# Optimization experiments

Hardware: AMD Instinct MI355X
Metric: run time of the kernel (lower is better)

The kernel has to match this reference:

```python
import jax, jax.numpy as jnp
import numpy as np

B, T, D, H = 128, 256, 256, 1024
DEC_STEPS = 59


def _gates(g):
    # torch LSTM gate order: input, forget, cell(g), output
    i, f, gg, o = jnp.split(g, 4, axis=-1)
    return jax.nn.sigmoid(i), jax.nn.sigmoid(f), jnp.tanh(gg), jax.nn.sigmoid(o)


def _cell(x, h, c, W_ih, W_hh, b_ih, b_hh):
    g = x @ W_ih.T + b_ih + h @ W_hh.T + b_hh
    i, f, gg, o = _gates(g)
    c = f * c + i * gg
    h = o * jnp.tanh(c)
    return h, c


def _layer(x, W_ih, W_hh, b_ih, b_hh):
    # x: [B, T, Din] -> outputs [B, T, H], final (h, c)
    b, hdim = x.shape[0], W_hh.shape[1]
    xp = jnp.einsum('btd,gd->btg', x, W_ih) + b_ih  # precompute input proj [B,T,4H]

    def step(carry, xt):
        h, c = carry
        g = xt + h @ W_hh.T + b_hh
        i, f, gg, o = _gates(g)
        c = f * c + i * gg
        h = o * jnp.tanh(c)
        return (h, c), h

    h0 = jnp.zeros((b, hdim), x.dtype)
    (hT, cT), hs = jax.lax.scan(step, (h0, h0), jnp.swapaxes(xp, 0, 1))
    return jnp.swapaxes(hs, 0, 1), hT, cT


def setup_inputs() -> dict:
    key = jax.random.key(0)
    ks = jax.random.split(key, 12)
    s = 1.0 / np.sqrt(H)
    u = lambda k, shape: jax.random.uniform(k, shape, jnp.float32, -s, s)
    return {
        'x': jax.random.normal(ks[0], (B, T, D), jnp.float32),
        'W_ih0': u(ks[1], (4 * H, D)),
        'W_hh0': u(ks[2], (4 * H, H)),
        'b_ih0': u(ks[3], (4 * H,)),
        'b_hh0': u(ks[4], (4 * H,)),
        'W_ih1': u(ks[5], (4 * H, H)),
        'W_hh1': u(ks[6], (4 * H, H)),
        'b_ih1': u(ks[7], (4 * H,)),
        'b_hh1': u(ks[8], (4 * H,)),
        'W_lin': u(ks[9], (D, H)),
        'b_lin': u(ks[10], (D,)),
    }


def reference(x, W_ih0, W_hh0, b_ih0, b_hh0, W_ih1, W_hh1, b_ih1, b_hh1, W_lin, b_lin):
    out0, h0, c0 = _layer(x, W_ih0, W_hh0, b_ih0, b_hh0)
    out1, h1, c1 = _layer(out0, W_ih1, W_hh1, b_ih1, b_hh1)
    y_last = out1[:, -1, :] @ W_lin.T + b_lin  # [B, D]

    def dec(carry, _):
        h0_, c0_, h1_, c1_, y = carry
        h0_, c0_ = _cell(y, h0_, c0_, W_ih0, W_hh0, b_ih0, b_hh0)
        h1_, c1_ = _cell(h0_, h1_, c1_, W_ih1, W_hh1, b_ih1, b_hh1)
        y = h1_ @ W_lin.T + b_lin
        return (h0_, c0_, h1_, c1_, y), y

    _, ys = jax.lax.scan(dec, (h0, c0, h1, c1, y_last), None, length=DEC_STEPS)
    ys = jnp.swapaxes(ys, 0, 1)  # [B, 59, D]
    # original returns y[:, T-1:, :] => last prefix prediction + 59 decoded steps
    return jnp.concatenate([y_last[:, None, :], ys], axis=1)  # [B, 60, D]
```

## Files before the change

kernel.cpp:

```cpp
#include <hip/hip_runtime.h>
#include <hip/hip_bf16.h>
#include <cstdint>


typedef _Float16 half_t;
typedef _Float16 half8 __attribute__((ext_vector_type(8)));
typedef float float4v __attribute__((ext_vector_type(4)));
typedef int int32x4_t __attribute__((ext_vector_type(4)));
typedef float float32x4_t __attribute__((ext_vector_type(4)));

__device__ float32x4_t llvm_amdgcn_raw_buffer_load_fp32x4(
    int32x4_t srsrc, int voffset, int soffset, int aux)
    __asm("llvm.amdgcn.raw.buffer.load.v4f32");

#define AUX_SC1 16

union SrdU { int32x4_t v; struct { const void* p; unsigned nr, fl; } s; };
__device__ __forceinline__ int32x4_t make_srd(const void* p) {
  SrdU u; u.s.p = p; u.s.nr = 0xFFFFFFFFu; u.s.fl = 0x00020000u; return u.v;
}

__device__ __forceinline__ unsigned poll4(const int* p) {
  union { float32x4_t f; int i[4]; } u;
  u.f = llvm_amdgcn_raw_buffer_load_fp32x4(make_srd(p), 0, 0, AUX_SC1);
  unsigned m = 0;
  if (u.i[0] >= 16) m |= 1u;
  if (u.i[1] >= 16) m |= 2u;
  if (u.i[2] >= 16) m |= 4u;
  if (u.i[3] >= 16) m |= 8u;
  return m;
}

__device__ __forceinline__ void wait8(const int* f) {
  for (;;) {
    unsigned m = poll4(f) | (poll4(f + 4) << 4);
    if (m == 0xFFu) return;
    __builtin_amdgcn_s_sleep(2);
  }
}

__device__ __forceinline__ void flag_add(int* p) {
  __hip_atomic_fetch_add(p, 1, __ATOMIC_RELAXED, __HIP_MEMORY_SCOPE_AGENT);
}

__device__ __forceinline__ void gate(const int* f, int tid) {
  if (tid == 0) wait8(f);
  asm volatile("" ::: "memory");
  __builtin_amdgcn_s_barrier();
  asm volatile("" ::: "memory");
}

__device__ __forceinline__ float sigm_(float x) { return 1.0f / (1.0f + __expf(-x)); }
__device__ __forceinline__ float tanh_(float x) {
  float ax = fabsf(x);
  float e = __expf(-2.0f * ax);
  float t = (1.0f - e) / (1.0f + e);
  return x < 0.0f ? -t : t;
}

#define MFMA16(a, b, c) __builtin_amdgcn_mfma_f32_16x16x32_f16(a, b, c, 0, 0, 0)


template <int NC>
__device__ __forceinline__ void issue_chunks(const half_t* __restrict__ A, int ro,
                                             half8 (&a0)[NC][4], half8 (&a1)[NC][4]) {
#pragma unroll
  for (int c = 0; c < NC; ++c)
#pragma unroll
    for (int k4 = 0; k4 < 4; ++k4) {
      const half_t* ap = A + (c * 16 + k4 * 4) * 1024 + ro;
      a0[c][k4] = *(const half8*)ap;
      a1[c][k4] = *(const half8*)(ap + 128);
    }
}

template <int NC>
__device__ __forceinline__ void consume_chunks(const half8 (&a0)[NC][4],
                                               const half8 (&a1)[NC][4],
                                               const half_t* __restrict__ W, int kk0,
                                               int lq, int lrow, float4v acc[2][2]) {
#pragma unroll
  for (int c = 0; c < NC; ++c)
#pragma unroll
    for (int k4 = 0; k4 < 4; ++k4) {
      const half_t* bp = W + (kk0 + c * 4 + k4) * 1024 + lq * 256 + lrow * 8;
      half8 b0 = *(const half8*)bp;
      half8 b1 = *(const half8*)(bp + 128);
      acc[0][0] = MFMA16(a0[c][k4], b0, acc[0][0]);
      acc[0][1] = MFMA16(a0[c][k4], b1, acc[0][1]);
      acc[1][0] = MFMA16(a1[c][k4], b0, acc[1][0]);
      acc[1][1] = MFMA16(a1[c][k4], b1, acc[1][1]);
    }
}

__device__ __forceinline__ void stream_main8(const half_t* __restrict__ A,
                                             const half_t* __restrict__ W, int kk0,
                                             int ro, int lq, int lrow,
                                             float4v acc[2][2],
                                             half8 (&a0)[4][4], half8 (&a1)[4][4]) {
#pragma unroll
  for (int c = 0; c < 8; ++c) {
#pragma unroll
    for (int k4 = 0; k4 < 4; ++k4) {
      const half_t* bp = W + (kk0 + c * 4 + k4) * 1024 + lq * 256 + lrow * 8;
      half8 b0 = *(const half8*)bp;
      half8 b1 = *(const half8*)(bp + 128);
      acc[0][0] = MFMA16(a0[c & 3][k4], b0, acc[0][0]);
      acc[0][1] = MFMA16(a0[c & 3][k4], b1, acc[0][1]);
      acc[1][0] = MFMA16(a1[c & 3][k4], b0, acc[1][0]);
      acc[1][1] = MFMA16(a1[c & 3][k4], b1, acc[1][1]);
    }
    if (c < 4) {
#pragma unroll
      for (int k4 = 0; k4 < 4; ++k4) {
        const half_t* ap = A + ((c + 4) * 16 + k4 * 4) * 1024 + ro;
        a0[c][k4] = *(const half8*)ap;
        a1[c][k4] = *(const half8*)(ap + 128);
      }
    }
  }
}

__device__ __forceinline__ void stream8(const half_t* __restrict__ A,
                                        const half_t* __restrict__ W, int kk0,
                                        int ro, int lq, int lrow, float4v acc[2][2]) {
  half8 a0[4][4], a1[4][4];
  issue_chunks<4>(A, ro, a0, a1);
  stream_main8(A, W, kk0, ro, lq, lrow, acc, a0, a1);
}

__device__ __forceinline__ void stream8_pre2(const half_t* __restrict__ A,
                                             const half_t* __restrict__ W, int kk0,
                                             const half8 (&xa0)[2][4],
                                             const half8 (&xa1)[2][4],
                                             int ro, int lq, int lrow,
                                             float4v acc[2][2]) {
  half8 a0[4][4], a1[4][4];
  issue_chunks<4>(A, ro, a0, a1);
  consume_chunks<2>(xa0, xa1, W, 0, lq, lrow, acc);
  stream_main8(A, W, kk0, ro, lq, lrow, acc, a0, a1);
}

__device__ __forceinline__ void epi_gates(
    float4v acc[2][2], int tile, const float* __restrict__ biasArr,
    float c[2][2], half_t* hTile, half_t* __restrict__ hDst, int tid) {
  const int l = tid & 63, rg = tid >> 6;
  const int lrow = l & 15, lq = l >> 4, q = l & 3, a = lrow >> 2;
#pragma unroll
  for (int m = 0; m < 2; ++m)
#pragma unroll
    for (int nf = 0; nf < 2; ++nf) {
      const float bias = biasArr[tile * 32 + nf * 16 + lrow];
      float gi = 0.f, gf = 0.f, gg = 0.f, go = 0.f;
#pragma unroll
      for (int r = 0; r < 4; ++r) {
        float x = acc[m][nf][r] + bias;
        float t1 = __shfl_xor(x, 1);
        float t2 = __shfl_xor(x, 2);
        float t3 = __shfl_xor(x, 3);
        if (r == q) {
          gi = (q == 0) ? x : (q == 1 ? t1 : (q == 2 ? t2 : t3));
          gf = (q == 1) ? x : (q == 0 ? t1 : (q == 3 ? t2 : t3));
          gg = (q == 2) ? x : (q == 3 ? t1 : (q == 0 ? t2 : t3));
          go = (q == 3) ? x : (q == 2 ? t1 : (q == 1 ? t2 : t3));
        }
      }
      const int row = rg * 32 + m * 16 + lq * 4 + q;
      const int ju = nf * 4 + a;
      float iv = sigm_(gi), fv = sigm_(gf), gv = tanh_(gg), ov = sigm_(go);
      float cnew = fv * c[m][nf] + iv * gv;
      c[m][nf] = cnew;
      hTile[row * 8 + ju] = (half_t)(ov * tanh_(cnew));
    }
  __syncthreads();
  if (tid < 128) {
    const unsigned long long* s = (const unsigned long long*)(hTile + tid * 8);
    unsigned long long v0 = s[0], v1 = s[1];
    unsigned long long* d = (unsigned long long*)(hDst + tid * 8);
    __hip_atomic_store(d, v0, __ATOMIC_RELAXED, __HIP_MEMORY_SCOPE_AGENT);
    __hip_atomic_store(d + 1, v1, __ATOMIC_RELAXED, __HIP_MEMORY_SCOPE_AGENT);
  }
}

__device__ __forceinline__ void epi_y(
    float4v acc[2][2], int ytile, int i, const float* __restrict__ biasY,
    float* __restrict__ out, int tid) {
  const int l = tid & 63, rg = tid >> 6;
  const int lrow = l & 15, lq = l >> 4;
#pragma unroll
  for (int m = 0; m < 2; ++m)
#pragma unroll
    for (int nf = 0; nf < 2; ++nf) {
      const int d = ytile * 32 + nf * 16 + lrow;
      const float b = biasY[d];
#pragma unroll
      for (int r = 0; r < 4; ++r) {
        const int row = rg * 32 + m * 16 + lq * 4 + r;
        out[(long)row * 15360 + i * 256 + d] = acc[m][nf][r] + b;
      }
    }
}

__device__ __forceinline__ void loadW(const half_t* __restrict__ src,
                                      half_t* dst, int halves, int tid) {
  for (int i = tid * 8; i < halves; i += 2048)
    *(uint4*)(dst + i) = *(const uint4*)(src + i);
}

#define ZACC2 float4v acc[2][2]; { float4v z = {0.f, 0.f, 0.f, 0.f}; \
  acc[0][0] = z; acc[0][1] = z; acc[1][0] = z; acc[1][1] = z; }

__global__ void __launch_bounds__(256, 1) k_lstm(
    const half_t* __restrict__ S0, const half_t* __restrict__ S1,
    const half_t* __restrict__ SD, const half_t* __restrict__ SY,
    const half_t* __restrict__ XH,
    half_t* __restrict__ H0, half_t* __restrict__ H1,
    const float* __restrict__ B0P, const float* __restrict__ B1P,
    const float* __restrict__ BD0P, float* __restrict__ out, int* FLG) {
  __shared__ char smem[133120];
  half_t* ldsW = (half_t*)smem;
  half_t* hTile = (half_t*)(smem + 131072);
  const int w = blockIdx.x, tid = threadIdx.x;
  const int l = tid & 63, rg = tid >> 6;
  const int lrow = l & 15, lq = l >> 4;
  const int ro = (rg * 32 + lrow) * 8 + lq * 1024;
  float c2[2][2] = {{0.f, 0.f}, {0.f, 0.f}};
#define SLOTP(base, idx) ((base) + (long)(idx) * 131072)

  if (w < 128) {
    const int g = w >> 4;
    loadW(S0 + (long)w * 40960, ldsW, 40960, tid);
    __syncthreads();
    for (int s = 0; s < 256; ++s) {
      ZACC2;
      half8 xa0[2][4], xa1[2][4];
      issue_chunks<2>(XH + (long)s * 32768, ro, xa0, xa1);
      if (s >= 1) gate(FLG + (s - 1) * 32, tid);
      stream8_pre2(SLOTP(H0, s), ldsW, 8, xa0, xa1, ro, lq, lrow, acc);
      epi_gates(acc, w, B0P, c2, hTile, SLOTP(H0, s + 1) + w * 1024, tid);
      __syncthreads();
      if (tid == 0) flag_add(FLG + s * 32 + g);
    }
    __syncthreads();
    loadW(SD + (long)w * 65536, ldsW, 65536, tid);
    __syncthreads();
    for (int i = 0; i < 59; ++i) {
      ZACC2;
      gate(FLG + (255 + i) * 32, tid);
      stream8(SLOTP(H0, 256 + i), ldsW, 32, ro, lq, lrow, acc);
      gate(FLG + (256 + i) * 32 + 8, tid);
      stream8(SLOTP(H1, 256 + i), ldsW, 0, ro, lq, lrow, acc);
      epi_gates(acc, w, BD0P, c2, hTile, SLOTP(H0, 257 + i) + w * 1024, tid);
      __syncthreads();
      if (tid == 0) flag_add(FLG + (256 + i) * 32 + g);
    }
  } else {
    const int bw = w - 128, g = bw >> 4;
    loadW(S1 + (long)bw * 65536, ldsW, 65536, tid);
    __syncthreads();
    for (int s = 1; s <= 256; ++s) {
      ZACC2;
      if (s >= 2) gate(FLG + (s - 1) * 32 + 8, tid);
      stream8(SLOTP(H1, s - 1), ldsW, 32, ro, lq, lrow, acc);
      gate(FLG + (s - 1) * 32, tid);
      stream8(SLOTP(H0, s), ldsW, 0, ro, lq, lrow, acc);
      epi_gates(acc, bw, B1P, c2, hTile, SLOTP(H1, s) + bw * 1024, tid);
      __syncthreads();
      if (tid == 0) flag_add(FLG + s * 32 + 8 + g);
    }
    for (int i = 0; i < 59; ++i) {
      ZACC2;
      gate(FLG + (256 + i) * 32 + 8, tid);
      stream8(SLOTP(H1, 256 + i), ldsW, 32, ro, lq, lrow, acc);
      gate(FLG + (256 + i) * 32, tid);
      stream8(SLOTP(H0, 257 + i), ldsW, 0, ro, lq, lrow, acc);
      epi_gates(acc, bw, B1P, c2, hTile, SLOTP(H1, 257 + i) + bw * 1024, tid);
      __syncthreads();
      if (tid == 0) flag_add(FLG + (257 + i) * 32 + 8 + g);
    }
  }

  for (int j = w; j < 480; j += 256) {
    const int i = j >> 3, t = j & 7;
    ZACC2;
    gate(FLG + (256 + i) * 32 + 8, tid);
    stream8(SLOTP(H1, 256 + i), SY + (long)t * 32768, 0, ro, lq, lrow, acc);
    epi_y(acc, t, i, BD0P + 4096, out, tid);
  }
#undef SLOTP
}


__global__ void k_cvt_x(const float* __restrict__ x, half_t* __restrict__ XH) {
  int idx = blockIdx.x * 256 + threadIdx.x;
  int t = idx >> 12;
  int kb = (idx >> 7) & 31;
  int r = idx & 127;
  const float* src = x + ((long)((r << 8) + t)) * 256 + kb * 8;
  float4 v0 = *(const float4*)src;
  float4 v1 = *(const float4*)(src + 4);
  half_t tmp[8] = {(half_t)v0.x, (half_t)v0.y, (half_t)v0.z, (half_t)v0.w,
                   (half_t)v1.x, (half_t)v1.y, (half_t)v1.z, (half_t)v1.w};
  *(uint4*)(XH + (long)t * 32768 + kb * 1024 + r * 8) = *(const uint4*)tmp;
}

__global__ void k_pack32(const float* __restrict__ A, int KA,
                         const float* __restrict__ Bsrc,
                         half_t* __restrict__ dst, int KT32, int skipA) {
  int idx = blockIdx.x * 256 + threadIdx.x;
  int nn = idx & 31;
  int lq = (idx >> 5) & 3;
  int t2 = idx >> 7;
  int kk = t2 % KT32;
  int tile = t2 / KT32;
  if (tile >= 128) return;
  int k = kk * 32 + lq * 8;
  int rp = tile * 32 + nn;
  int r = ((rp & 3) << 10) + (rp >> 2);
  const float* src;
  if (k < KA) {
    if (skipA) return;
    src = A + (long)r * KA + k;
  } else {
    src = Bsrc + (long)r * 1024 + (k - KA);
  }
  float4 v0 = *(const float4*)src;
  float4 v1 = *(const float4*)(src + 4);
  half_t tmp[8] = {(half_t)v0.x, (half_t)v0.y, (half_t)v0.z, (half_t)v0.w,
                   (half_t)v1.x, (half_t)v1.y, (half_t)v1.z, (half_t)v1.w};
  *(uint4*)(dst + (long)tile * (KT32 * 1024) + kk * 1024 + lq * 256 + nn * 8) =
      *(const uint4*)tmp;
}

__global__ void k_pack_y32(const float* __restrict__ Wlin,
                           half_t* __restrict__ SY) {
  int idx = blockIdx.x * 256 + threadIdx.x;
  int nn = idx & 31;
  int lq = (idx >> 5) & 3;
  int kk = (idx >> 7) & 31;
  int tile = idx >> 12;
  int d = tile * 32 + nn;
  int k = kk * 32 + lq * 8;
  const float* src = Wlin + (long)d * 1024 + k;
  float4 v0 = *(const float4*)src;
  float4 v1 = *(const float4*)(src + 4);
  half_t tmp[8] = {(half_t)v0.x, (half_t)v0.y, (half_t)v0.z, (half_t)v0.w,
                   (half_t)v1.x, (half_t)v1.y, (half_t)v1.z, (half_t)v1.w};
  *(uint4*)(SY + (long)tile * 32768 + kk * 1024 + lq * 256 + nn * 8) =
      *(const uint4*)tmp;
}

__global__ void k_bias_simple(const float* bi0, const float* bh0,
                              const float* bi1, const float* bh1,
                              const float* blin, float* b0p, float* b1p,
                              float* bD0p) {
  int rp = blockIdx.x * blockDim.x + threadIdx.x;
  if (rp < 4096) {
    int r = ((rp & 3) << 10) + (rp >> 2);
    b0p[rp] = bi0[r] + bh0[r];
    b1p[rp] = bi1[r] + bh1[r];
  } else if (rp < 4352) {
    bD0p[rp] = blin[rp - 4096];
  }
}

__global__ void k_bias_dot(const float* __restrict__ Wih0,
                           const float* __restrict__ blin,
                           const float* __restrict__ bi0,
                           const float* __restrict__ bh0,
                           float* __restrict__ bD0p) {
  int wv = threadIdx.x >> 6, l = threadIdx.x & 63;
  int r = blockIdx.x * 4 + wv;
  float s = 0.f;
#pragma unroll
  for (int c = 0; c < 4; ++c) s += Wih0[r * 256 + c * 64 + l] * blin[c * 64 + l];
#pragma unroll
  for (int o = 32; o >= 1; o >>= 1) s += __shfl_xor(s, o);
  if (l == 0) {
    int rp = ((r & 1023) << 2) | (r >> 10);
    bD0p[rp] = bi0[r] + bh0[r] + s;
  }
}

__global__ void k_weff(const float* __restrict__ Wih0,
                       const float* __restrict__ Wlin,
                       half_t* __restrict__ SD) {
  __shared__ float At[64][65];
  __shared__ float Bt[64][65];
  const int rt = blockIdx.x, jt = blockIdx.y;
  const int tid = threadIdx.x;
  const int tx = tid & 15, ty = tid >> 4;
  float acc[4][4] = {};
  for (int k0 = 0; k0 < 256; k0 += 64) {
    __syncthreads();
#pragma unroll
    for (int i = 0; i < 16; ++i) {
      int lin = tid + 256 * i;
      int rr = lin >> 6, kk = lin & 63;
      At[rr][kk] = Wih0[(rt * 64 + rr) * 256 + k0 + kk];
      Bt[rr][kk] = Wlin[(k0 + rr) * 1024 + jt * 64 + kk];
    }
    __syncthreads();
    for (int kk = 0; kk < 64; ++kk) {
      float a[4], b[4];
#pragma unroll
      for (int i = 0; i < 4; ++i) a[i] = At[ty * 4 + i][kk];
#pragma unroll
      for (int i = 0; i < 4; ++i) b[i] = Bt[kk][tx * 4 + i];
#pragma unroll
      for (int i = 0; i < 4; ++i)
#pragma unroll
        for (int jx = 0; jx < 4; ++jx) acc[i][jx] += a[i] * b[jx];
    }
  }
#pragma unroll
  for (int i = 0; i < 4; ++i) {
    int r = rt * 64 + ty * 4 + i;
    int rp = ((r & 1023) << 2) | (r >> 10);
    int tile = rp >> 5, nn = rp & 31;
#pragma unroll
    for (int jx = 0; jx < 4; ++jx) {
      int j = jt * 64 + tx * 4 + jx;
      SD[(long)tile * 65536 + (j >> 5) * 1024 + ((j >> 3) & 3) * 256 + nn * 8 +
         (j & 7)] = (half_t)acc[i][jx];
    }
  }
}


extern "C" void kernel_launch(void* const* d_in, const int* in_sizes, int n_in,
                              void* d_out, int out_size, void* d_ws, size_t ws_size,
                              hipStream_t stream) {
  (void)in_sizes; (void)n_in; (void)out_size; (void)ws_size;
  const float* x    = (const float*)d_in[0];
  const float* Wih0 = (const float*)d_in[1];
  const float* Whh0 = (const float*)d_in[2];
  const float* bi0  = (const float*)d_in[3];
  const float* bh0  = (const float*)d_in[4];
  const float* Wih1 = (const float*)d_in[5];
  const float* Whh1 = (const float*)d_in[6];
  const float* bi1  = (const float*)d_in[7];
  const float* bh1  = (const float*)d_in[8];
  const float* Wlin = (const float*)d_in[9];
  const float* blin = (const float*)d_in[10];
  float* out = (float*)d_out;
  char* ws = (char*)d_ws;

  half_t* S0  = (half_t*)(ws + 0);
  half_t* S1  = (half_t*)(ws + 10485760);
  half_t* SD  = (half_t*)(ws + 27262976);
  half_t* SY  = (half_t*)(ws + 44040192);
  half_t* XH  = (half_t*)(ws + 44564480);
  float*  B0P = (float*)(ws + 61341696);
  float*  B1P = (float*)(ws + 61358080);
  float*  BD0P= (float*)(ws + 61374464);
  int*    FLG = (int*)(ws + 61391872);
  half_t* H0  = (half_t*)(ws + 61432320);
  half_t* H1  = (half_t*)(ws + 145318400);

  hipMemsetAsync(ws + 61391872, 0, 302592, stream);
  hipMemsetAsync(H1, 0, 262144, stream);

  k_cvt_x<<<4096, 256, 0, stream>>>(x, XH);
  k_bias_simple<<<17, 256, 0, stream>>>(bi0, bh0, bi1, bh1, blin, B0P, B1P, BD0P);
  k_bias_dot<<<1024, 256, 0, stream>>>(Wih0, blin, bi0, bh0, BD0P);
  k_pack32<<<2560, 256, 0, stream>>>(Wih0, 256, Whh0, S0, 40, 0);
  k_pack32<<<4096, 256, 0, stream>>>(Wih1, 1024, Whh1, S1, 64, 0);
  k_pack32<<<4096, 256, 0, stream>>>(nullptr, 1024, Whh0, SD, 64, 1);
  k_pack_y32<<<128, 256, 0, stream>>>(Wlin, SY);
  k_weff<<<dim3(64, 16), 256, 0, stream>>>(Wih0, Wlin, SD);

  k_lstm<<<256, 256, 0, stream>>>(S0, S1, SD, SY, XH, H0, H1,
                                  B0P, B1P, BD0P, out, FLG);
}
```

Measured before the change: 5.521 ms.

## Replace per-group atomic counters with per-block byte flags and early input MFMA

The cross-block step flags change from eight atomic-increment counters per layer-step to a 128-byte record per layer-step. Each block stores one byte with a relaxed store, and the waiter checks all 128 bytes with eight vector buffer loads against 0x01010101. In layer 0, the input-projection MFMAs now run before the gate wait, so that work overlaps the dependency stall. The flag area moves after H1, and H0 slot 0 is now zeroed explicitly. The cost is more polling loads per check and reliance on byte-store visibility ordering relative to the H writes.

```diff
diff --git a/kernel.cpp b/kernel.cpp
--- a/kernel.cpp
+++ b/kernel.cpp
@@ -20,31 +20,31 @@
   SrdU u; u.s.p = p; u.s.nr = 0xFFFFFFFFu; u.s.fl = 0x00020000u; return u.v;
 }
 
-__device__ __forceinline__ unsigned poll4(const int* p) {
-  union { float32x4_t f; int i[4]; } u;
-  u.f = llvm_amdgcn_raw_buffer_load_fp32x4(make_srd(p), 0, 0, AUX_SC1);
-  unsigned m = 0;
-  if (u.i[0] >= 16) m |= 1u;
-  if (u.i[1] >= 16) m |= 2u;
-  if (u.i[2] >= 16) m |= 4u;
-  if (u.i[3] >= 16) m |= 8u;
-  return m;
-}
-
-__device__ __forceinline__ void wait8(const int* f) {
-  for (;;) {
-    unsigned m = poll4(f) | (poll4(f + 4) << 4);
-    if (m == 0xFFu) return;
-    __builtin_amdgcn_s_sleep(2);
-  }
-}
-
-__device__ __forceinline__ void flag_add(int* p) {
-  __hip_atomic_fetch_add(p, 1, __ATOMIC_RELAXED, __HIP_MEMORY_SCOPE_AGENT);
+__device__ __forceinline__ bool poll128(const int* p) {
+  union { float32x4_t f; int i[4]; } u[8];
+  int32x4_t srd = make_srd(p);
+#pragma unroll
+  for (int j = 0; j < 8; ++j)
+    u[j].f = llvm_amdgcn_raw_buffer_load_fp32x4(srd, j * 16, 0, AUX_SC1);
+  int ok = 1;
+#pragma unroll
+  for (int j = 0; j < 8; ++j)
+#pragma unroll
+    for (int k = 0; k < 4; ++k) ok &= (u[j].i[k] == 0x01010101);
+  return ok != 0;
+}
+
+__device__ __forceinline__ void wait128(const int* f) {
+  while (!poll128(f)) __builtin_amdgcn_s_sleep(2);
+}
+
+__device__ __forceinline__ void flag_set(int* recp, int idx) {
+  __hip_atomic_store((char*)recp + idx, (char)1, __ATOMIC_RELAXED,
+                     __HIP_MEMORY_SCOPE_AGENT);
 }
 
 __device__ __forceinline__ void gate(const int* f, int tid) {
-  if (tid == 0) wait8(f);
+  if (tid == 0) wait128(f);
   asm volatile("" ::: "memory");
   __builtin_amdgcn_s_barrier();
   asm volatile("" ::: "memory");
@@ -126,18 +126,6 @@
                                         int ro, int lq, int lrow, float4v acc[2][2]) {
   half8 a0[4][4], a1[4][4];
   issue_chunks<4>(A, ro, a0, a1);
-  stream_main8(A, W, kk0, ro, lq, lrow, acc, a0, a1);
-}
-
-__device__ __forceinline__ void stream8_pre2(const half_t* __restrict__ A,
-                                             const half_t* __restrict__ W, int kk0,
-                                             const half8 (&xa0)[2][4],
-                                             const half8 (&xa1)[2][4],
-                                             int ro, int lq, int lrow,
-                                             float4v acc[2][2]) {
-  half8 a0[4][4], a1[4][4];
-  issue_chunks<4>(A, ro, a0, a1);
-  consume_chunks<2>(xa0, xa1, W, 0, lq, lrow, acc);
   stream_main8(A, W, kk0, ro, lq, lrow, acc, a0, a1);
 }
 
@@ -216,7 +204,7 @@
     const half_t* __restrict__ XH,
     half_t* __restrict__ H0, half_t* __restrict__ H1,
     const float* __restrict__ B0P, const float* __restrict__ B1P,
-    const float* __restrict__ BD0P, float* __restrict__ out, int* FLG) {
+    const float* __restrict__ BD0P, float* __restrict__ out, int* FLGB) {
   __shared__ char smem[133120];
   half_t* ldsW = (half_t*)smem;
   half_t* hTile = (half_t*)(smem + 131072);
@@ -226,67 +214,69 @@
   const int ro = (rg * 32 + lrow) * 8 + lq * 1024;
   float c2[2][2] = {{0.f, 0.f}, {0.f, 0.f}};
 #define SLOTP(base, idx) ((base) + (long)(idx) * 131072)
+#define REC(s, lay) (FLGB + ((((s) * 2 + (lay))) << 6))
 
   if (w < 128) {
-    const int g = w >> 4;
     loadW(S0 + (long)w * 40960, ldsW, 40960, tid);
     __syncthreads();
     for (int s = 0; s < 256; ++s) {
       ZACC2;
       half8 xa0[2][4], xa1[2][4];
       issue_chunks<2>(XH + (long)s * 32768, ro, xa0, xa1);
-      if (s >= 1) gate(FLG + (s - 1) * 32, tid);
-      stream8_pre2(SLOTP(H0, s), ldsW, 8, xa0, xa1, ro, lq, lrow, acc);
+      consume_chunks<2>(xa0, xa1, ldsW, 0, lq, lrow, acc);
+      if (s >= 1) gate(REC(s - 1, 0), tid);
+      stream8(SLOTP(H0, s), ldsW, 8, ro, lq, lrow, acc);
       epi_gates(acc, w, B0P, c2, hTile, SLOTP(H0, s + 1) + w * 1024, tid);
       __syncthreads();
-      if (tid == 0) flag_add(FLG + s * 32 + g);
+      if (tid == 0) flag_set(REC(s, 0), w);
     }
     __syncthreads();
     loadW(SD + (long)w * 65536, ldsW, 65536, tid);
     __syncthreads();
     for (int i = 0; i < 59; ++i) {
       ZACC2;
-      gate(FLG + (255 + i) * 32, tid);
+      gate(REC(255 + i, 0), tid);
       stream8(SLOTP(H0, 256 + i), ldsW, 32, ro, lq, lrow, acc);
-      gate(FLG + (256 + i) * 32 + 8, tid);
+      gate(REC(256 + i, 1), tid);
       stream8(SLOTP(H1, 256 + i), ldsW, 0, ro, lq, lrow, acc);
       epi_gates(acc, w, BD0P, c2, hTile, SLOTP(H0, 257 + i) + w * 1024, tid);
       __syncthreads();
-      if (tid == 0) flag_add(FLG + (256 + i) * 32 + g);
+      if (tid == 0) flag_set(REC(256 + i, 0), w);
     }
   } else {
-    const int bw = w - 128, g = bw >> 4;
+    const int bw = w - 128;
     loadW(S1 + (long)bw * 65536, ldsW, 65536, tid);
     __syncthreads();
     for (int s = 1; s <= 256; ++s) {
       ZACC2;
-      if (s >= 2) gate(FLG + (s - 1) * 32 + 8, tid);
+      if (s >= 2) gate(REC(s - 1, 1), tid);
       stream8(SLOTP(H1, s - 1), ldsW, 32, ro, lq, lrow, acc);
-      gate(FLG + (s - 1) * 32, tid);
+      gate(REC(s - 1, 0), tid);
       stream8(SLOTP(H0, s), ldsW, 0, ro, lq, lrow, acc);
       epi_gates(acc, bw, B1P, c2, hTile, SLOTP(H1, s) + bw * 1024, tid);
       __syncthreads();
-      if (tid == 0) flag_add(FLG + s * 32 + 8 + g);
+      if (tid == 0) flag_set(REC(s, 1), bw);
     }
     for (int i = 0; i < 59; ++i) {
       ZACC2;
-      gate(FLG + (256 + i) * 32 + 8, tid);
+      gate(REC(256 + i, 1), tid);
       stream8(SLOTP(H1, 256 + i), ldsW, 32, ro, lq, lrow, acc);
-      gate(FLG + (256 + i) * 32, tid);
+      gate(REC(256 + i, 0), tid);
       stream8(SLOTP(H0, 257 + i), ldsW, 0, ro, lq, lrow, acc);
       epi_gates(acc, bw, B1P, c2, hTile, SLOTP(H1, 257 + i) + bw * 1024, tid);
       __syncthreads();
-      if (tid == 0) flag_add(FLG + (257 + i) * 32 + 8 + g);
+      if (tid == 0) flag_set(REC(257 + i, 1), bw);
     }
   }
 
   for (int j = w; j < 480; j += 256) {
     const int i = j >> 3, t = j & 7;
     ZACC2;
-    gate(FLG + (256 + i) * 32 + 8, tid);
+    gate(REC(256 + i, 1), tid);
     stream8(SLOTP(H1, 256 + i), SY + (long)t * 32768, 0, ro, lq, lrow, acc);
     epi_y(acc, t, i, BD0P + 4096, out, tid);
   }
+#undef REC
 #undef SLOTP
 }
 
@@ -454,11 +444,12 @@
   float*  B0P = (float*)(ws + 61341696);
   float*  B1P = (float*)(ws + 61358080);
   float*  BD0P= (float*)(ws + 61374464);
-  int*    FLG = (int*)(ws + 61391872);
   half_t* H0  = (half_t*)(ws + 61432320);
   half_t* H1  = (half_t*)(ws + 145318400);
-
-  hipMemsetAsync(ws + 61391872, 0, 302592, stream);
+  int*    FLGB= (int*)(ws + 145318400 + (long)316 * 262144);
+
+  hipMemsetAsync(FLGB, 0, 163840, stream);
+  hipMemsetAsync(H0, 0, 262144, stream);
   hipMemsetAsync(H1, 0, 262144, stream);
 
   k_cvt_x<<<4096, 256, 0, stream>>>(x, XH);
@@ -471,5 +462,5 @@
   k_weff<<<dim3(64, 16), 256, 0, stream>>>(Wih0, Wlin, SD);
 
   k_lstm<<<256, 256, 0, stream>>>(S0, S1, SD, SY, XH, H0, H1,
-                                  B0P, B1P, BD0P, out, FLG);
-}
+                                  B0P, B1P, BD0P, out, FLGB);
+}
```

Result: slower. 5.807 ms (+5.2%).

## Replace block-wide flag gates with per-wave, per-chunk dependency polling

Applied to the files above, without the earlier changes.

Inter-block step flags are split per row-group (wave) and per producer chunk. Each wave now waits only for the specific K-chunk it is about to load instead of one thread waiting on all eight producers followed by a block barrier. This lets loads and MFMAs on already-ready chunks start while other producers finish, and it peels the first layer-0 step. It adds more flag atomics and polling traffic, plus an extra barrier in the epilogue.

```diff
diff --git a/kernel.cpp b/kernel.cpp
--- a/kernel.cpp
+++ b/kernel.cpp
@@ -31,23 +31,24 @@
   return m;
 }
 
-__device__ __forceinline__ void wait8(const int* f) {
-  for (;;) {
-    unsigned m = poll4(f) | (poll4(f + 4) << 4);
-    if (m == 0xFFu) return;
-    __builtin_amdgcn_s_sleep(2);
-  }
+__device__ __forceinline__ unsigned peek8(const int* f) {
+  return poll4(f) | (poll4(f + 4) << 4);
+}
+
+__device__ __forceinline__ void wait_chunk(const int* f, int c, unsigned& got) {
+  if (!((got >> c) & 1)) {
+    const int b = c & ~3;
+    for (;;) {
+      got |= poll4(f + b) << b;
+      if ((got >> c) & 1) break;
+      __builtin_amdgcn_s_sleep(2);
+    }
+  }
+  asm volatile("" ::: "memory");
 }
 
 __device__ __forceinline__ void flag_add(int* p) {
   __hip_atomic_fetch_add(p, 1, __ATOMIC_RELAXED, __HIP_MEMORY_SCOPE_AGENT);
-}
-
-__device__ __forceinline__ void gate(const int* f, int tid) {
-  if (tid == 0) wait8(f);
-  asm volatile("" ::: "memory");
-  __builtin_amdgcn_s_barrier();
-  asm volatile("" ::: "memory");
 }
 
 __device__ __forceinline__ float sigm_(float x) { return 1.0f / (1.0f + __expf(-x)); }
@@ -61,17 +62,37 @@
 #define MFMA16(a, b, c) __builtin_amdgcn_mfma_f32_16x16x32_f16(a, b, c, 0, 0, 0)
 
 
+__device__ __forceinline__ void issue_chunk(const half_t* __restrict__ A, int c,
+                                            int ro, half8 (&a0)[4], half8 (&a1)[4]) {
+#pragma unroll
+  for (int k4 = 0; k4 < 4; ++k4) {
+    const half_t* ap = A + (c * 16 + k4 * 4) * 1024 + ro;
+    a0[k4] = *(const half8*)ap;
+    a1[k4] = *(const half8*)(ap + 128);
+  }
+}
+
+__device__ __forceinline__ void consume_chunk(const half8 (&a0)[4],
+                                              const half8 (&a1)[4],
+                                              const half_t* __restrict__ W, int kk0,
+                                              int lq, int lrow, float4v acc[2][2]) {
+#pragma unroll
+  for (int k4 = 0; k4 < 4; ++k4) {
+    const half_t* bp = W + (kk0 + k4) * 1024 + lq * 256 + lrow * 8;
+    half8 b0 = *(const half8*)bp;
+    half8 b1 = *(const half8*)(bp + 128);
+    acc[0][0] = MFMA16(a0[k4], b0, acc[0][0]);
+    acc[0][1] = MFMA16(a0[k4], b1, acc[0][1]);
+    acc[1][0] = MFMA16(a1[k4], b0, acc[1][0]);
+    acc[1][1] = MFMA16(a1[k4], b1, acc[1][1]);
+  }
+}
+
 template <int NC>
 __device__ __forceinline__ void issue_chunks(const half_t* __restrict__ A, int ro,
                                              half8 (&a0)[NC][4], half8 (&a1)[NC][4]) {
 #pragma unroll
-  for (int c = 0; c < NC; ++c)
-#pragma unroll
-    for (int k4 = 0; k4 < 4; ++k4) {
-      const half_t* ap = A + (c * 16 + k4 * 4) * 1024 + ro;
-      a0[c][k4] = *(const half8*)ap;
-      a1[c][k4] = *(const half8*)(ap + 128);
-    }
+  for (int c = 0; c < NC; ++c) issue_chunk(A, c, ro, a0[c], a1[c]);
 }
 
 template <int NC>
@@ -81,64 +102,53 @@
                                                int lq, int lrow, float4v acc[2][2]) {
 #pragma unroll
   for (int c = 0; c < NC; ++c)
-#pragma unroll
-    for (int k4 = 0; k4 < 4; ++k4) {
-      const half_t* bp = W + (kk0 + c * 4 + k4) * 1024 + lq * 256 + lrow * 8;
-      half8 b0 = *(const half8*)bp;
-      half8 b1 = *(const half8*)(bp + 128);
-      acc[0][0] = MFMA16(a0[c][k4], b0, acc[0][0]);
-      acc[0][1] = MFMA16(a0[c][k4], b1, acc[0][1]);
-      acc[1][0] = MFMA16(a1[c][k4], b0, acc[1][0]);
-      acc[1][1] = MFMA16(a1[c][k4], b1, acc[1][1]);
-    }
-}
-
-__device__ __forceinline__ void stream_main8(const half_t* __restrict__ A,
-                                             const half_t* __restrict__ W, int kk0,
-                                             int ro, int lq, int lrow,
-                                             float4v acc[2][2],
-                                             half8 (&a0)[4][4], half8 (&a1)[4][4]) {
+    consume_chunk(a0[c], a1[c], W, kk0 + c * 4, lq, lrow, acc);
+}
+
+__device__ __forceinline__ void stream8g(const half_t* __restrict__ A,
+                                         const half_t* __restrict__ W, int kk0,
+                                         const int* f, unsigned got,
+                                         int ro, int lq, int lrow, float4v acc[2][2]) {
+  half8 a0[4][4], a1[4][4];
+#pragma unroll
+  for (int c = 0; c < 4; ++c) {
+    wait_chunk(f, c, got);
+    issue_chunk(A, c, ro, a0[c], a1[c]);
+  }
 #pragma unroll
   for (int c = 0; c < 8; ++c) {
-#pragma unroll
-    for (int k4 = 0; k4 < 4; ++k4) {
-      const half_t* bp = W + (kk0 + c * 4 + k4) * 1024 + lq * 256 + lrow * 8;
-      half8 b0 = *(const half8*)bp;
-      half8 b1 = *(const half8*)(bp + 128);
-      acc[0][0] = MFMA16(a0[c & 3][k4], b0, acc[0][0]);
-      acc[0][1] = MFMA16(a0[c & 3][k4], b1, acc[0][1]);
-      acc[1][0] = MFMA16(a1[c & 3][k4], b0, acc[1][0]);
-      acc[1][1] = MFMA16(a1[c & 3][k4], b1, acc[1][1]);
-    }
+    consume_chunk(a0[c & 3], a1[c & 3], W, kk0 + c * 4, lq, lrow, acc);
     if (c < 4) {
-#pragma unroll
-      for (int k4 = 0; k4 < 4; ++k4) {
-        const half_t* ap = A + ((c + 4) * 16 + k4 * 4) * 1024 + ro;
-        a0[c][k4] = *(const half8*)ap;
-        a1[c][k4] = *(const half8*)(ap + 128);
-      }
-    }
-  }
-}
-
-__device__ __forceinline__ void stream8(const half_t* __restrict__ A,
-                                        const half_t* __restrict__ W, int kk0,
-                                        int ro, int lq, int lrow, float4v acc[2][2]) {
+      wait_chunk(f, c + 4, got);
+      issue_chunk(A, c + 4, ro, a0[c & 3], a1[c & 3]);
+    }
+  }
+}
+
+__device__ __forceinline__ void stream_l0p(const half_t* __restrict__ XHs,
+                                           const half_t* __restrict__ A,
+                                           const half_t* __restrict__ W,
+                                           const int* f, int ro, int lq, int lrow,
+                                           float4v acc[2][2]) {
+  half8 xa0[2][4], xa1[2][4];
+  issue_chunks<2>(XHs, ro, xa0, xa1);
+  unsigned got = peek8(f);
   half8 a0[4][4], a1[4][4];
-  issue_chunks<4>(A, ro, a0, a1);
-  stream_main8(A, W, kk0, ro, lq, lrow, acc, a0, a1);
-}
-
-__device__ __forceinline__ void stream8_pre2(const half_t* __restrict__ A,
-                                             const half_t* __restrict__ W, int kk0,
-                                             const half8 (&xa0)[2][4],
-                                             const half8 (&xa1)[2][4],
-                                             int ro, int lq, int lrow,
-                                             float4v acc[2][2]) {
-  half8 a0[4][4], a1[4][4];
-  issue_chunks<4>(A, ro, a0, a1);
-  consume_chunks<2>(xa0, xa1, W, 0, lq, lrow, acc);
-  stream_main8(A, W, kk0, ro, lq, lrow, acc, a0, a1);
+#pragma unroll
+  for (int c = 0; c < 4; ++c) {
+    wait_chunk(f, c, got);
+    issue_chunk(A, c, ro, a0[c], a1[c]);
+  }
+  consume_chunk(xa0[0], xa1[0], W, 0, lq, lrow, acc);
+  consume_chunk(xa0[1], xa1[1], W, 4, lq, lrow, acc);
+#pragma unroll
+  for (int c = 0; c < 8; ++c) {
+    consume_chunk(a0[c & 3], a1[c & 3], W, 8 + c * 4, lq, lrow, acc);
+    if (c < 4) {
+      wait_chunk(f, c + 4, got);
+      issue_chunk(A, c + 4, ro, a0[c & 3], a1[c & 3]);
+    }
+  }
 }
 
 __device__ __forceinline__ void epi_gates(
@@ -146,6 +156,7 @@
     float c[2][2], half_t* hTile, half_t* __restrict__ hDst, int tid) {
   const int l = tid & 63, rg = tid >> 6;
   const int lrow = l & 15, lq = l >> 4, q = l & 3, a = lrow >> 2;
+  __syncthreads();
 #pragma unroll
   for (int m = 0; m < 2; ++m)
 #pragma unroll
@@ -216,7 +227,7 @@
     const half_t* __restrict__ XH,
     half_t* __restrict__ H0, half_t* __restrict__ H1,
     const float* __restrict__ B0P, const float* __restrict__ B1P,
-    const float* __restrict__ BD0P, float* __restrict__ out, int* FLG) {
+    const float* __restrict__ BD0P, float* __restrict__ out, int* FLGB) {
   __shared__ char smem[133120];
   half_t* ldsW = (half_t*)smem;
   half_t* hTile = (half_t*)(smem + 131072);
@@ -226,33 +237,42 @@
   const int ro = (rg * 32 + lrow) * 8 + lq * 1024;
   float c2[2][2] = {{0.f, 0.f}, {0.f, 0.f}};
 #define SLOTP(base, idx) ((base) + (long)(idx) * 131072)
+#define FREC(s, lay, rr) (FLGB + ((((s) * 2 + (lay)) * 4 + (rr)) << 5))
 
   if (w < 128) {
     const int g = w >> 4;
     loadW(S0 + (long)w * 40960, ldsW, 40960, tid);
     __syncthreads();
-    for (int s = 0; s < 256; ++s) {
+    {
       ZACC2;
       half8 xa0[2][4], xa1[2][4];
-      issue_chunks<2>(XH + (long)s * 32768, ro, xa0, xa1);
-      if (s >= 1) gate(FLG + (s - 1) * 32, tid);
-      stream8_pre2(SLOTP(H0, s), ldsW, 8, xa0, xa1, ro, lq, lrow, acc);
+      issue_chunks<2>(XH, ro, xa0, xa1);
+      consume_chunks<2>(xa0, xa1, ldsW, 0, lq, lrow, acc);
+      epi_gates(acc, w, B0P, c2, hTile, SLOTP(H0, 1) + w * 1024, tid);
+      __syncthreads();
+      if ((tid & 63) == 0) flag_add(FREC(0, 0, rg) + g);
+    }
+    for (int s = 1; s < 256; ++s) {
+      ZACC2;
+      stream_l0p(XH + (long)s * 32768, SLOTP(H0, s), ldsW, FREC(s - 1, 0, rg),
+                 ro, lq, lrow, acc);
       epi_gates(acc, w, B0P, c2, hTile, SLOTP(H0, s + 1) + w * 1024, tid);
       __syncthreads();
-      if (tid == 0) flag_add(FLG + s * 32 + g);
+      if ((tid & 63) == 0) flag_add(FREC(s, 0, rg) + g);
     }
     __syncthreads();
     loadW(SD + (long)w * 65536, ldsW, 65536, tid);
     __syncthreads();
     for (int i = 0; i < 59; ++i) {
       ZACC2;
-      gate(FLG + (255 + i) * 32, tid);
-      stream8(SLOTP(H0, 256 + i), ldsW, 32, ro, lq, lrow, acc);
-      gate(FLG + (256 + i) * 32 + 8, tid);
-      stream8(SLOTP(H1, 256 + i), ldsW, 0, ro, lq, lrow, acc);
+      const int* fO = FREC(255 + i, 0, rg);
+      const int* fF = FREC(256 + i, 1, rg);
+      unsigned gotF = peek8(fF);
+      stream8g(SLOTP(H0, 256 + i), ldsW, 32, fO, peek8(fO), ro, lq, lrow, acc);
+      stream8g(SLOTP(H1, 256 + i), ldsW, 0, fF, gotF, ro, lq, lrow, acc);
       epi_gates(acc, w, BD0P, c2, hTile, SLOTP(H0, 257 + i) + w * 1024, tid);
       __syncthreads();
-      if (tid == 0) flag_add(FLG + (256 + i) * 32 + g);
+      if ((tid & 63) == 0) flag_add(FREC(256 + i, 0, rg) + g);
     }
   } else {
     const int bw = w - 128, g = bw >> 4;
@@ -260,33 +280,39 @@
     __syncthreads();
     for (int s = 1; s <= 256; ++s) {
       ZACC2;
-      if (s >= 2) gate(FLG + (s - 1) * 32 + 8, tid);
-      stream8(SLOTP(H1, s - 1), ldsW, 32, ro, lq, lrow, acc);
-      gate(FLG + (s - 1) * 32, tid);
-      stream8(SLOTP(H0, s), ldsW, 0, ro, lq, lrow, acc);
+      const int* fF = FREC(s - 1, 0, rg);
+      unsigned gotF = peek8(fF);
+      if (s >= 2) {
+        const int* fO = FREC(s - 1, 1, rg);
+        stream8g(SLOTP(H1, s - 1), ldsW, 32, fO, peek8(fO), ro, lq, lrow, acc);
+      }
+      stream8g(SLOTP(H0, s), ldsW, 0, fF, gotF, ro, lq, lrow, acc);
       epi_gates(acc, bw, B1P, c2, hTile, SLOTP(H1, s) + bw * 1024, tid);
       __syncthreads();
-      if (tid == 0) flag_add(FLG + s * 32 + 8 + g);
+      if ((tid & 63) == 0) flag_add(FREC(s, 1, rg) + g);
     }
     for (int i = 0; i < 59; ++i) {
       ZACC2;
-      gate(FLG + (256 + i) * 32 + 8, tid);
-      stream8(SLOTP(H1, 256 + i), ldsW, 32, ro, lq, lrow, acc);
-      gate(FLG + (256 + i) * 32, tid);
-      stream8(SLOTP(H0, 257 + i), ldsW, 0, ro, lq, lrow, acc);
+      const int* fO = FREC(256 + i, 1, rg);
+      const int* fF = FREC(256 + i, 0, rg);
+      unsigned gotF = peek8(fF);
+      stream8g(SLOTP(H1, 256 + i), ldsW, 32, fO, peek8(fO), ro, lq, lrow, acc);
+      stream8g(SLOTP(H0, 257 + i), ldsW, 0, fF, gotF, ro, lq, lrow, acc);
       epi_gates(acc, bw, B1P, c2, hTile, SLOTP(H1, 257 + i) + bw * 1024, tid);
       __syncthreads();
-      if (tid == 0) flag_add(FLG + (257 + i) * 32 + 8 + g);
+      if ((tid & 63) == 0) flag_add(FREC(257 + i, 1, rg) + g);
     }
   }
 
   for (int j = w; j < 480; j += 256) {
     const int i = j >> 3, t = j & 7;
     ZACC2;
-    gate(FLG + (256 + i) * 32 + 8, tid);
-    stream8(SLOTP(H1, 256 + i), SY + (long)t * 32768, 0, ro, lq, lrow, acc);
+    const int* f = FREC(256 + i, 1, rg);
+    stream8g(SLOTP(H1, 256 + i), SY + (long)t * 32768, 0, f, peek8(f),
+             ro, lq, lrow, acc);
     epi_y(acc, t, i, BD0P + 4096, out, tid);
   }
+#undef FREC
 #undef SLOTP
 }
 
@@ -454,11 +480,12 @@
   float*  B0P = (float*)(ws + 61341696);
   float*  B1P = (float*)(ws + 61358080);
   float*  BD0P= (float*)(ws + 61374464);
-  int*    FLG = (int*)(ws + 61391872);
   half_t* H0  = (half_t*)(ws + 61432320);
   half_t* H1  = (half_t*)(ws + 145318400);
-
-  hipMemsetAsync(ws + 61391872, 0, 302592, stream);
+  int*    FLGB= (int*)(ws + 145318400 + (long)316 * 262144);
+
+  hipMemsetAsync(FLGB, 0, 327680, stream);
+  hipMemsetAsync(H0, 0, 262144, stream);
   hipMemsetAsync(H1, 0, 262144, stream);
 
   k_cvt_x<<<4096, 256, 0, stream>>>(x, XH);
@@ -471,5 +498,5 @@
   k_weff<<<dim3(64, 16), 256, 0, stream>>>(Wih0, Wlin, SD);
 
   k_lstm<<<256, 256, 0, stream>>>(S0, S1, SD, SY, XH, H0, H1,
-                                  B0P, B1P, BD0P, out, FLG);
-}
+                                  B0P, B1P, BD0P, out, FLGB);
+}
```

Result: faster. 4.648 ms (-15.8%).
